# Optimization experiments

Hardware: AMD Instinct MI355X
Metric: run time of the kernel (lower is better)

## Reference

```python
import jax, jax.numpy as jnp
import numpy as np

B, T, H, NH = 4, 1024, 1024, 16
HS = H // NH
FF = 4 * H
EPS = 1e-5


def setup_inputs() -> dict:
    key = jax.random.key(0)
    ks = jax.random.split(key, 12)
    s = 0.02
    inp = {
        "x": jax.random.normal(ks[0], (B, T, H), jnp.float32),
        # attention projections, stored as [in, out] so y = x @ W + b
        "Wq": jax.random.normal(ks[1], (H, H), jnp.float32) * s,
        "bq": jnp.zeros((H,), jnp.float32),
        "Wk": jax.random.normal(ks[2], (H, H), jnp.float32) * s,
        "bk": jnp.zeros((H,), jnp.float32),
        "Wv": jax.random.normal(ks[3], (H, H), jnp.float32) * s,
        "bv": jnp.zeros((H,), jnp.float32),
        "Wo": jax.random.normal(ks[4], (H, H), jnp.float32) * s,
        "bo": jnp.zeros((H,), jnp.float32),
        # layernorms
        "ln1_w": jnp.ones((H,), jnp.float32),
        "ln1_b": jnp.zeros((H,), jnp.float32),
        "ln2_w": jnp.ones((H,), jnp.float32),
        "ln2_b": jnp.zeros((H,), jnp.float32),
        # MLP
        "Wfc": jax.random.normal(ks[5], (H, FF), jnp.float32) * s,
        "bfc": jnp.zeros((FF,), jnp.float32),
        "Wpr": jax.random.normal(ks[6], (FF, H), jnp.float32) * s,
        "bpr": jnp.zeros((H,), jnp.float32),
    }
    return inp


def _layernorm(x, w, b):
    mu = jnp.mean(x, axis=-1, keepdims=True)
    var = jnp.mean(jnp.square(x - mu), axis=-1, keepdims=True)
    return (x - mu) * jax.lax.rsqrt(var + EPS) * w + b


def _rope(x):
    # x: [B, nh, T, hs]; interleaved-pair RoPE, base 10000
    half = HS // 2
    inv_freq = 1.0 / (10000.0 ** (jnp.arange(half, dtype=jnp.float32) / half))
    ang = jnp.arange(T, dtype=jnp.float32)[:, None] * inv_freq[None, :]  # [T, half]
    cos, sin = jnp.cos(ang), jnp.sin(ang)
    xr = x.reshape(*x.shape[:-1], half, 2)
    x0, x1 = xr[..., 0], xr[..., 1]
    r0 = x0 * cos - x1 * sin
    r1 = x0 * sin + x1 * cos
    return jnp.stack([r0, r1], axis=-1).reshape(x.shape)


def _block(x, Wq, bq, Wk, bk, Wv, bv, Wo, bo, ln1_w, ln1_b, ln2_w, ln2_b, Wfc, bfc, Wpr, bpr):
    # --- attention sub-block ---
    h1 = _layernorm(x, ln1_w, ln1_b)
    q = (h1 @ Wq + bq).reshape(B, T, NH, HS).transpose(0, 2, 1, 3)  # [B,nh,T,hs]
    k = (h1 @ Wk + bk).reshape(B, T, NH, HS).transpose(0, 2, 1, 3)
    v = (h1 @ Wv + bv).reshape(B, T, NH, HS).transpose(0, 2, 1, 3)
    q, k = _rope(q), _rope(k)
    scores = jnp.einsum('bhqd,bhkd->bhqk', q, k) / jnp.sqrt(jnp.float32(HS))
    attn = jax.nn.softmax(scores, axis=-1)
    # NOTE: original applies the causal mask AFTER softmax (multiplicative, no renorm)
    causal = jnp.tril(jnp.ones((T, T), jnp.float32))[None, None]
    attn = attn * causal
    out = jnp.einsum('bhqk,bhkd->bhqd', attn, v)
    out = out.transpose(0, 2, 1, 3).reshape(B, T, H)
    x = x + (out @ Wo + bo)
    # --- MLP sub-block ---
    h2 = _layernorm(x, ln2_w, ln2_b)
    m = jax.nn.gelu(h2 @ Wfc + bfc, approximate=False)
    x = x + (m @ Wpr + bpr)
    return x


def reference(x, Wq, bq, Wk, bk, Wv, bv, Wo, bo, ln1_w, ln1_b, ln2_w, ln2_b, Wfc, bfc, Wpr, bpr):
    return _block(x, Wq, bq, Wk, bk, Wv, bv, Wo, bo, ln1_w, ln1_b, ln2_w, ln2_b, Wfc, bfc, Wpr, bpr)
```

## Files before the change

### kernel.cpp

```cpp
#include <hip/hip_runtime.h>
#include <hip/hip_bf16.h>

typedef unsigned short u16;
typedef __attribute__((ext_vector_type(8))) short bf16x8;
typedef __attribute__((ext_vector_type(4))) float f32x4;
typedef __attribute__((ext_vector_type(4))) unsigned short u16x4;

#define B_  4
#define T_  1024
#define H_  1024
#define NH_ 16
#define HS_ 64
#define FF_ 4096
#define M_  (B_*T_)
#define QKV_S 3072

__device__ __forceinline__ u16 f2bf(float f){
  union { float f; unsigned u; } v; v.f = f;
  unsigned r = v.u + 0x7fffu + ((v.u >> 16) & 1u);
  return (u16)(r >> 16);
}
__device__ __forceinline__ float bf2f(u16 h){
  union { unsigned u; float f; } v; v.u = ((unsigned)h) << 16;
  return v.f;
}
__device__ __forceinline__ unsigned pack2bf(float a, float b){
  __hip_bfloat162 h = __float22bfloat162_rn(make_float2(a, b));
  union { __hip_bfloat162 h; unsigned u; } c; c.h = h;
  return c.u;
}

__device__ __forceinline__ void gload_lds16(const void* g, void* l){
  __builtin_amdgcn_global_load_lds(
      (const __attribute__((address_space(1))) unsigned int*)g,
      (__attribute__((address_space(3))) unsigned int*)l,
      16, 0, 0);
}

__device__ __forceinline__ void trans_tile(const float* __restrict__ W,
                                           u16* __restrict__ Wt, int K, int N,
                                           int k0, int n0, int tid)
{
  __shared__ u16 tile[64][68];
  #pragma unroll
  for (int it = 0; it < 4; ++it){
    int ci = tid + it * 256;
    int kr = ci >> 4, nc = ci & 15;
    float4 f = *(const float4*)(W + (size_t)(k0 + kr) * N + n0 + nc * 4);
    tile[kr][nc*4+0] = f2bf(f.x);
    tile[kr][nc*4+1] = f2bf(f.y);
    tile[kr][nc*4+2] = f2bf(f.z);
    tile[kr][nc*4+3] = f2bf(f.w);
  }
  __syncthreads();
  #pragma unroll
  for (int it = 0; it < 4; ++it){
    int co = tid + it * 256;
    int nr = co >> 4, kc = co & 15;
    u16x4 o;
    o[0] = tile[kc*4+0][nr];
    o[1] = tile[kc*4+1][nr];
    o[2] = tile[kc*4+2][nr];
    o[3] = tile[kc*4+3][nr];
    *(u16x4*)(Wt + (size_t)(n0 + nr) * K + k0 + kc * 4) = o;
  }
}

__global__ __launch_bounds__(256) void trans_qkvo_k(
    const float* __restrict__ Wq, const float* __restrict__ Wk,
    const float* __restrict__ Wv, const float* __restrict__ Wo,
    u16* __restrict__ WqkvT, u16* __restrict__ WoT)
{
  const int z = blockIdx.z;
  const float* src = (z == 0) ? Wq : (z == 1) ? Wk : (z == 2) ? Wv : Wo;
  u16* dst = (z == 3) ? WoT : (WqkvT + (size_t)z * 1024 * 1024);
  trans_tile(src, dst, H_, H_, blockIdx.y * 64, blockIdx.x * 64, threadIdx.x);
}

__global__ __launch_bounds__(256) void transpose_cvt(const float* __restrict__ W,
                                                     u16* __restrict__ Wt, int K, int N)
{
  trans_tile(W, Wt, K, N, blockIdx.y * 64, blockIdx.x * 64, threadIdx.x);
}

__global__ __launch_bounds__(256) void vtrans_k(const u16* __restrict__ qkv,
                                                u16* __restrict__ vtg)
{
  __shared__ u16 tile[64][72];
  const int bh = blockIdx.y, tt = blockIdx.x * 64;
  const int b = bh >> 4, h = bh & 15;
  const size_t src = (size_t)b * T_ * QKV_S + h * HS_ + 2048;
  const int tid = threadIdx.x;
  #pragma unroll
  for (int it = 0; it < 2; ++it){
    int ci = tid + it * 256;
    int r = ci >> 3, c = ci & 7;
    bf16x8 vvv = *(const bf16x8*)(qkv + src + (size_t)(tt + r) * QKV_S + c * 8);
    *(bf16x8*)&tile[r][c * 8] = vvv;
  }
  __syncthreads();
  #pragma unroll
  for (int it = 0; it < 2; ++it){
    int co = tid + it * 256;
    int d = co >> 3, c = co & 7;
    bf16x8 ov;
    #pragma unroll
    for (int j = 0; j < 8; ++j) ov[j] = (short)tile[c * 8 + j][d];
    *(bf16x8*)(vtg + (size_t)bh * HS_ * T_ + (size_t)d * T_ + tt + c * 8) = ov;
  }
}

__global__ void prep_small_k(const float* __restrict__ a, const float* __restrict__ b,
                             const float* __restrict__ c, float* __restrict__ o,
                             float* __restrict__ tab){
  int i = blockIdx.x * 256 + threadIdx.x;
  if (i < QKV_S){
    o[i] = (i < 1024) ? a[i] : (i < 2048) ? b[i - 1024] : c[i - 2048];
  } else {
    int j = i - QKV_S;
    if (j < T_ * 32){
      int t = j >> 5, f = j & 31;
      float inv = powf(10000.0f, -(float)f * (1.0f / 32.0f));
      float ang = (float)t * inv;
      tab[j*2+0] = cosf(ang);
      tab[j*2+1] = sinf(ang);
    }
  }
}

__global__ void rope_apply_k(u16* __restrict__ qkv, const float* __restrict__ tab){
  int i = blockIdx.x * blockDim.x + threadIdx.x;
  if (i >= B_*T_*NH_*32) return;
  int pr = i & 31;
  int nh = (i >> 5) & (NH_ - 1);
  int bt = i >> 9;
  int t  = bt & (T_ - 1);
  size_t idx = (size_t)bt * QKV_S + nh * HS_ + pr * 2;
  float c = tab[(t*32 + pr)*2], s = tab[(t*32 + pr)*2 + 1];
  const float qs = 0.125f * 1.44269504f;
  {
    float x0 = bf2f(qkv[idx]), x1 = bf2f(qkv[idx+1]);
    qkv[idx]   = f2bf((x0 * c - x1 * s) * qs);
    qkv[idx+1] = f2bf((x0 * s + x1 * c) * qs);
  }
  {
    float x0 = bf2f(qkv[idx+1024]), x1 = bf2f(qkv[idx+1025]);
    qkv[idx+1024] = f2bf(x0 * c - x1 * s);
    qkv[idx+1025] = f2bf(x0 * s + x1 * c);
  }
}

__global__ __launch_bounds__(256) void ln_kernel(const float* __restrict__ x,
    const float* __restrict__ w, const float* __restrict__ bgain,
    u16* __restrict__ out)
{
  const int row = blockIdx.x;
  const int t = threadIdx.x;
  float4 vv = ((const float4*)(x + (size_t)row * H_))[t];
  float s  = vv.x + vv.y + vv.z + vv.w;
  float s2 = vv.x*vv.x + vv.y*vv.y + vv.z*vv.z + vv.w*vv.w;
  #pragma unroll
  for (int mm = 1; mm < 64; mm <<= 1){ s += __shfl_xor(s, mm); s2 += __shfl_xor(s2, mm); }
  __shared__ float red[8];
  int wid = t >> 6;
  if ((t & 63) == 0){ red[wid] = s; red[4 + wid] = s2; }
  __syncthreads();
  s  = red[0] + red[1] + red[2] + red[3];
  s2 = red[4] + red[5] + red[6] + red[7];
  float mu  = s * (1.0f / H_);
  float var = s2 * (1.0f / H_) - mu * mu;
  float rin = rsqrtf(var + 1e-5f);
  float4 wv = ((const float4*)w)[t];
  float4 bv = ((const float4*)bgain)[t];
  u16x4 ov;
  ov[0] = f2bf((vv.x - mu) * rin * wv.x + bv.x);
  ov[1] = f2bf((vv.y - mu) * rin * wv.y + bv.y);
  ov[2] = f2bf((vv.z - mu) * rin * wv.z + bv.z);
  ov[3] = f2bf((vv.w - mu) * rin * wv.w + bv.w);
  ((u16x4*)(out + (size_t)row * H_))[t] = ov;
}

template<int EPI, int RING>
__global__ __launch_bounds__(512) void gemm_kernel(
    const u16* __restrict__ A, const u16* __restrict__ Bt,
    const float* __restrict__ bias, const float* __restrict__ res,
    void* __restrict__ Cout, int M, int N, int K)
{
  __shared__ __attribute__((aligned(16))) u16 As[RING][128 * 32];
  __shared__ __attribute__((aligned(16))) u16 Bs[RING][128 * 32];
  const int tid  = threadIdx.x;
  const int lane = tid & 63;
  const int wid  = tid >> 6;
  const int wm = wid >> 2, wn = wid & 3;
  const int lrow = lane & 15, lkg = lane >> 4;

  const int gx  = gridDim.x;
  const int nwg = gx * gridDim.y;
  const int wg  = blockIdx.y * gx + blockIdx.x;
  const int nx  = nwg >> 3;
  const int swz = (wg & 7) * nx + (wg >> 3);
  const int m0 = (swz / gx) * 128, n0 = (swz % gx) * 128;

  const int srow = tid >> 2;
  const int sdc  = tid & 3;
  const int scs  = sdc ^ ((srow >> 1) & 3);

  const u16* Arow = A  + (size_t)(m0 + srow) * K + scs * 8;
  const u16* Brow = Bt + (size_t)(n0 + srow) * K + scs * 8;
  const int dd = (srow * 4 + sdc) * 8;

  int aoff[4], boff[2];
  #pragma unroll
  for (int mi = 0; mi < 4; ++mi){
    int r = wm*64 + mi*16 + lrow;
    aoff[mi] = (r*4 + (lkg ^ ((r >> 1) & 3))) * 16;
  }
  #pragma unroll
  for (int ni = 0; ni < 2; ++ni){
    int r = wn*32 + ni*16 + lrow;
    boff[ni] = (r*4 + (lkg ^ ((r >> 1) & 3))) * 16;
  }

  f32x4 acc[4][2] = {};
  const int NT = K >> 5;
  constexpr int DIST = RING - 1;

  #pragma unroll
  for (int s = 0; s < DIST; ++s){
    gload_lds16(Arow + (s << 5), &As[s][dd]);
    gload_lds16(Brow + (s << 5), &Bs[s][dd]);
  }

  int rs = 0, wsl = DIST;
  for (int t = 0; t < NT; ++t){
    int cnt = NT - 1 - t; if (cnt > DIST - 1) cnt = DIST - 1;
    if (cnt >= 4)      asm volatile("s_waitcnt vmcnt(8)" ::: "memory");
    else if (cnt == 3) asm volatile("s_waitcnt vmcnt(6)" ::: "memory");
    else if (cnt == 2) asm volatile("s_waitcnt vmcnt(4)" ::: "memory");
    else if (cnt == 1) asm volatile("s_waitcnt vmcnt(2)" ::: "memory");
    else               asm volatile("s_waitcnt vmcnt(0)" ::: "memory");
    __builtin_amdgcn_s_barrier();

    const char* Ab = (const char*)&As[rs][0];
    const char* Bb = (const char*)&Bs[rs][0];
    rs = (rs + 1 == RING) ? 0 : rs + 1;

    bf16x8 af[4], bfr[2];
    #pragma unroll
    for (int mi = 0; mi < 4; ++mi)
      af[mi] = *(const bf16x8*)(Ab + aoff[mi]);
    #pragma unroll
    for (int ni = 0; ni < 2; ++ni)
      bfr[ni] = *(const bf16x8*)(Bb + boff[ni]);
    __builtin_amdgcn_sched_barrier(0);

    if (t + DIST < NT){
      int k0 = (t + DIST) << 5;
      gload_lds16(Arow + k0, &As[wsl][dd]);
      gload_lds16(Brow + k0, &Bs[wsl][dd]);
    }
    wsl = (wsl + 1 == RING) ? 0 : wsl + 1;

    #pragma unroll
    for (int mi = 0; mi < 4; ++mi)
      #pragma unroll
      for (int ni = 0; ni < 2; ++ni)
        acc[mi][ni] = __builtin_amdgcn_mfma_f32_16x16x32_bf16(af[mi], bfr[ni], acc[mi][ni], 0, 0, 0);
  }

  #pragma unroll
  for (int mi = 0; mi < 4; ++mi){
    #pragma unroll
    for (int ni = 0; ni < 2; ++ni){
      int col = n0 + wn*32 + ni*16 + lrow;
      float bv = bias[col];
      #pragma unroll
      for (int r = 0; r < 4; ++r){
        int row = m0 + wm*64 + mi*16 + lkg*4 + r;
        float v = acc[mi][ni][r] + bv;
        if (EPI == 1){
          float u = 0.7978845608f * v + 0.0356774081f * v * v * v;
          float e = exp2f(u * 2.8853900818f);
          v = v - v / (e + 1.0f);
        }
        if (EPI == 2){
          ((float*)Cout)[(size_t)row * N + col] = v + res[(size_t)row * N + col];
        } else {
          ((u16*)Cout)[(size_t)row * N + col] = f2bf(v);
        }
      }
    }
  }
}

__global__ __launch_bounds__(512, 4) void attn_kernel(
    const u16* __restrict__ qkv, const u16* __restrict__ vtg,
    u16* __restrict__ out)
{
  __shared__ u16 K_lds[3][64 * 64];
  __shared__ u16 VT_lds[3][64 * 64];
  __shared__ u16 P_lds[8][16 * 64];
  const int tid = threadIdx.x, lane = tid & 63, w = tid >> 6;
  const int lrow = lane & 15, lkg = lane >> 4;
  const int q0 = blockIdx.x * 128;
  const int bh = blockIdx.y, b = bh >> 4, h = bh & 15;
  const size_t baseq  = (size_t)b * T_ * QKV_S + h * HS_;
  const size_t basek  = baseq + 1024;
  const size_t basevt = (size_t)bh * HS_ * T_;
  const size_t baseo  = (size_t)b * T_ * H_ + h * HS_;
  const int qg = q0 + w * 16 + lrow;

  bf16x8 qa[2];
  {
    const u16* qp = qkv + baseq + (size_t)qg * QKV_S + lkg * 8;
    qa[0] = *(const bf16x8*)qp;
    qa[1] = *(const bf16x8*)(qp + 32);
  }

  const int r0 = tid >> 3, c0 = tid & 7, g0 = c0 ^ (r0 & 7);
  const u16* kap = qkv + basek + (size_t)r0 * QKV_S + g0 * 8;
  const u16* vap = vtg + basevt + (size_t)r0 * T_ + g0 * 8;
  const int kd = tid * 8;

  f32x4 o[4] = {};
  float mrun = -1e30f, lrun = 0.f;

  #pragma unroll
  for (int s = 0; s < 2; ++s){
    gload_lds16(kap + (size_t)s * 64 * QKV_S, &K_lds[s][kd]);
    gload_lds16(vap + s * 64,                 &VT_lds[s][kd]);
  }

  int rs = 0, wsl = 2;
  for (int t = 0; t < 16; ++t){
    const int kt = t << 6;
    if (t < 15) asm volatile("s_waitcnt vmcnt(2)" ::: "memory");
    else        asm volatile("s_waitcnt vmcnt(0)" ::: "memory");
    __builtin_amdgcn_s_barrier();
    __builtin_amdgcn_sched_barrier(0);

    if (t + 2 < 16){
      gload_lds16(kap + (size_t)(t + 2) * 64 * QKV_S, &K_lds[wsl][kd]);
      gload_lds16(vap + (t + 2) * 64,                 &VT_lds[wsl][kd]);
    }
    wsl = (wsl + 1 == 3) ? 0 : wsl + 1;

    const u16* Kc  = K_lds[rs];
    const u16* VTc = VT_lds[rs];
    rs = (rs + 1 == 3) ? 0 : rs + 1;

    f32x4 s[4];
    __builtin_amdgcn_s_setprio(1);
    #pragma unroll
    for (int mi = 0; mi < 4; ++mi){
      f32x4 c = {};
      #pragma unroll
      for (int ss = 0; ss < 2; ++ss){
        int r = mi * 16 + lrow;
        int off = r * 128 + (((ss * 4 + lkg) ^ (r & 7)) * 16);
        bf16x8 kb = *(const bf16x8*)((const char*)Kc + off);
        c = __builtin_amdgcn_mfma_f32_16x16x32_bf16(kb, qa[ss], c, 0, 0, 0);
      }
      s[mi] = c;
    }
    __builtin_amdgcn_s_setprio(0);

    float mt = fmaxf(fmaxf(fmaxf(s[0][0], s[0][1]), fmaxf(s[0][2], s[0][3])),
                     fmaxf(fmaxf(s[1][0], s[1][1]), fmaxf(s[1][2], s[1][3])));
    mt = fmaxf(mt, fmaxf(fmaxf(fmaxf(s[2][0], s[2][1]), fmaxf(s[2][2], s[2][3])),
                         fmaxf(fmaxf(s[3][0], s[3][1]), fmaxf(s[3][2], s[3][3]))));
    mt = fmaxf(mt, __shfl_xor(mt, 16));
    mt = fmaxf(mt, __shfl_xor(mt, 32));
    if (!__all(mt <= mrun + 8.f)){
      float mnew = fmaxf(mrun, mt);
      float fsc = exp2f(mrun - mnew);
      lrun *= fsc;
      #pragma unroll
      for (int nf = 0; nf < 4; ++nf){
        #pragma unroll
        for (int r = 0; r < 4; ++r) o[nf][r] *= fsc;
      }
      mrun = mnew;
    }

    float p[16];
    float ls = 0.f;
    #pragma unroll
    for (int mi = 0; mi < 4; ++mi){
      #pragma unroll
      for (int r = 0; r < 4; ++r){
        int key = kt + mi * 16 + lkg * 4 + r;
        float pv = exp2f(s[mi][r] - mrun);
        ls += pv;
        p[mi * 4 + r] = (key <= qg) ? pv : 0.f;
      }
    }
    ls += __shfl_xor(ls, 16);
    ls += __shfl_xor(ls, 32);
    lrun += ls;

    if (kt <= q0 + w * 16 + 15){
      char* pbase = (char*)&P_lds[w][0];
      const int rx = (lrow & 7) << 4;
      #pragma unroll
      for (int mi = 0; mi < 4; ++mi){
        uint2 pk;
        pk.x = pack2bf(p[mi*4+0], p[mi*4+1]);
        pk.y = pack2bf(p[mi*4+2], p[mi*4+3]);
        *(uint2*)(pbase + (lrow * 128 + ((mi * 32 + lkg * 8) ^ rx))) = pk;
      }
      __builtin_amdgcn_s_setprio(1);
      #pragma unroll
      for (int ss = 0; ss < 2; ++ss){
        bf16x8 pb = *(const bf16x8*)(pbase + (lrow * 128 + ((ss * 64 + lkg * 16) ^ rx)));
        #pragma unroll
        for (int nfd = 0; nfd < 4; ++nfd){
          int d = nfd * 16 + lrow;
          int off = d * 128 + (((ss * 4 + lkg) ^ (d & 7)) * 16);
          bf16x8 vb = *(const bf16x8*)((const char*)VTc + off);
          o[nfd] = __builtin_amdgcn_mfma_f32_16x16x32_bf16(vb, pb, o[nfd], 0, 0, 0);
        }
      }
      __builtin_amdgcn_s_setprio(0);
    }
  }

  float rl = 1.0f / lrun;
  #pragma unroll
  for (int nfd = 0; nfd < 4; ++nfd){
    uint2 ov;
    ov.x = pack2bf(o[nfd][0] * rl, o[nfd][1] * rl);
    ov.y = pack2bf(o[nfd][2] * rl, o[nfd][3] * rl);
    *(uint2*)(out + baseo + (size_t)qg * H_ + nfd * 16 + lkg * 4) = ov;
  }
}

extern "C" void kernel_launch(void* const* d_in, const int* in_sizes, int n_in,
                              void* d_out, int out_size, void* d_ws, size_t ws_size,
                              hipStream_t stream)
{
  (void)in_sizes; (void)n_in; (void)out_size; (void)ws_size;
  const float* x    = (const float*)d_in[0];
  const float* Wq   = (const float*)d_in[1];
  const float* bq   = (const float*)d_in[2];
  const float* Wk   = (const float*)d_in[3];
  const float* bk   = (const float*)d_in[4];
  const float* Wv   = (const float*)d_in[5];
  const float* bv   = (const float*)d_in[6];
  const float* Wo   = (const float*)d_in[7];
  const float* bo   = (const float*)d_in[8];
  const float* ln1w = (const float*)d_in[9];
  const float* ln1b = (const float*)d_in[10];
  const float* ln2w = (const float*)d_in[11];
  const float* ln2b = (const float*)d_in[12];
  const float* Wfc  = (const float*)d_in[13];
  const float* bfc  = (const float*)d_in[14];
  const float* Wpr  = (const float*)d_in[15];
  const float* bpr  = (const float*)d_in[16];

  char* ws = (char*)d_ws;
  u16*  WqkvT = (u16*)(ws + ((size_t) 0 << 20));
  u16*  WoT   = (u16*)(ws + ((size_t) 6 << 20));
  u16*  WfcT  = (u16*)(ws + ((size_t) 8 << 20));
  u16*  WprT  = (u16*)(ws + ((size_t)16 << 20));
  u16*  h1    = (u16*)(ws + ((size_t)24 << 20));
  u16*  qkvb  = (u16*)(ws + ((size_t)32 << 20));
  float* x1   = (float*)(ws + ((size_t)32 << 20));
  u16*  h2    = (u16*)(ws + ((size_t)48 << 20));
  float* bqkv = (float*)(ws + ((size_t)56 << 20));
  float* rtab = (float*)(ws + ((size_t)56 << 20) + (64 << 10));
  u16*  vtg   = (u16*)(ws + ((size_t)57 << 20));
  u16*  mb    = (u16*)(ws + ((size_t)56 << 20));
  u16*  attnout = h1;

  dim3 blk(256);
  dim3 gblk(512);

  trans_qkvo_k<<<dim3(H_/64, H_/64, 4), blk, 0, stream>>>(Wq, Wk, Wv, Wo, WqkvT, WoT);
  transpose_cvt<<<dim3(FF_/64, H_/64),  blk, 0, stream>>>(Wfc, WfcT, H_,  FF_);
  transpose_cvt<<<dim3(H_/64,  FF_/64), blk, 0, stream>>>(Wpr, WprT, FF_, H_);
  prep_small_k<<<dim3((QKV_S + T_*32 + 255)/256), blk, 0, stream>>>(bq, bk, bv, bqkv, rtab);

  ln_kernel<<<dim3(M_), blk, 0, stream>>>(x, ln1w, ln1b, h1);
  gemm_kernel<0,3><<<dim3(QKV_S/128, M_/128), gblk, 0, stream>>>(h1, WqkvT, bqkv, nullptr, qkvb, M_, QKV_S, H_);
  rope_apply_k<<<dim3((B_*T_*NH_*32)/256), blk, 0, stream>>>(qkvb, rtab);
  vtrans_k<<<dim3(T_/64, B_*NH_), blk, 0, stream>>>(qkvb, vtg);
  attn_kernel<<<dim3(T_/128, B_*NH_), dim3(512), 0, stream>>>(qkvb, vtg, attnout);
  gemm_kernel<2,6><<<dim3(H_/128, M_/128), gblk, 0, stream>>>(attnout, WoT, bo, x, x1, M_, H_, H_);
  ln_kernel<<<dim3(M_), blk, 0, stream>>>(x1, ln2w, ln2b, h2);
  gemm_kernel<1,3><<<dim3(FF_/128, M_/128), gblk, 0, stream>>>(h2, WfcT, bfc, nullptr, mb, M_, FF_, H_);
  gemm_kernel<2,6><<<dim3(H_/128, M_/128), gblk, 0, stream>>>(mb, WprT, bpr, x1, (float*)d_out, M_, H_, FF_);
}
```

Measured before the change: 254.0 us.

## Add 128x256-tile GEMM with vectorized bf16 epilogue for QKV and FC layers

Adds a new GEMM kernel whose workgroup tile is 128x256 instead of 128x128. Each of its 8 waves computes a 64x64 sub-tile and the kernel uses a 3-stage LDS ring with K-step 32. It also adds a workgroup-index swizzle and an epilogue that adds bias as float4 and writes packed bf16x4 stores. The QKV and FC GEMMs now use it, which is meant to raise arithmetic intensity per byte loaded and cut global-load traffic for the wider-N matrices. The cost is more LDS and registers per workgroup and fewer workgroups in the grid, which may hurt occupancy or wave balance.

```diff
diff --git a/kernel.cpp b/kernel.cpp
--- a/kernel.cpp
+++ b/kernel.cpp
@@ -293,6 +293,125 @@
   }
 }
 
+template<int EPI>
+__global__ __launch_bounds__(512, 4) void gemm256_kernel(
+    const u16* __restrict__ A, const u16* __restrict__ Bt,
+    const float* __restrict__ bias,
+    void* __restrict__ Cout, int M, int N, int K)
+{
+  __shared__ __attribute__((aligned(16))) u16 As[3][128 * 32];
+  __shared__ __attribute__((aligned(16))) u16 Bs[3][256 * 32];
+  const int tid  = threadIdx.x;
+  const int lane = tid & 63;
+  const int wid  = tid >> 6;
+  const int wm = wid >> 2, wn = wid & 3;
+  const int lrow = lane & 15, lkg = lane >> 4;
+
+  const int gx  = gridDim.x;
+  const int nwg = gx * gridDim.y;
+  const int wg  = blockIdx.y * gx + blockIdx.x;
+  const int nx  = nwg >> 3;
+  const int swz = (wg & 7) * nx + (wg >> 3);
+  const int m0 = (swz / gx) * 128, n0 = (swz % gx) * 256;
+
+  const int srow = tid >> 2;
+  const int sdc  = tid & 3;
+  const int scs  = sdc ^ ((srow >> 1) & 3);
+  const u16* Asrc  = A  + (size_t)(m0 + srow) * K + scs * 8;
+  const u16* Bsrc0 = Bt + (size_t)(n0 + srow) * K + scs * 8;
+  const u16* Bsrc1 = Bsrc0 + (size_t)128 * K;
+  const int dA  = (srow * 4 + sdc) * 8;
+  const int dB1 = dA + 128 * 32;
+
+  int aoff[4], boff[4];
+  #pragma unroll
+  for (int mi = 0; mi < 4; ++mi){
+    int r = wm*64 + mi*16 + lrow;
+    aoff[mi] = (r*4 + (lkg ^ ((r >> 1) & 3))) * 16;
+  }
+  #pragma unroll
+  for (int ni = 0; ni < 4; ++ni){
+    int r = wn*64 + ni*16 + lrow;
+    boff[ni] = (r*4 + (lkg ^ ((r >> 1) & 3))) * 16;
+  }
+
+  f32x4 acc[4][4] = {};
+  const int NT = K >> 5;
+
+  #pragma unroll
+  for (int s = 0; s < 2; ++s){
+    gload_lds16(Asrc  + (s << 5), &As[s][dA]);
+    gload_lds16(Bsrc0 + (s << 5), &Bs[s][dA]);
+    gload_lds16(Bsrc1 + (s << 5), &Bs[s][dB1]);
+  }
+
+  int rs = 0, wsl = 2;
+  for (int t = 0; t < NT; ++t){
+    if (t < NT - 1) asm volatile("s_waitcnt vmcnt(3)" ::: "memory");
+    else            asm volatile("s_waitcnt vmcnt(0)" ::: "memory");
+    __builtin_amdgcn_s_barrier();
+
+    const char* Ab = (const char*)&As[rs][0];
+    const char* Bb = (const char*)&Bs[rs][0];
+    rs = (rs + 1 == 3) ? 0 : rs + 1;
+
+    bf16x8 af[4], bfr[4];
+    #pragma unroll
+    for (int mi = 0; mi < 4; ++mi)
+      af[mi] = *(const bf16x8*)(Ab + aoff[mi]);
+    #pragma unroll
+    for (int ni = 0; ni < 4; ++ni)
+      bfr[ni] = *(const bf16x8*)(Bb + boff[ni]);
+    __builtin_amdgcn_sched_barrier(0);
+
+    if (t + 2 < NT){
+      int k0 = (t + 2) << 5;
+      gload_lds16(Asrc  + k0, &As[wsl][dA]);
+      gload_lds16(Bsrc0 + k0, &Bs[wsl][dA]);
+      gload_lds16(Bsrc1 + k0, &Bs[wsl][dB1]);
+    }
+    wsl = (wsl + 1 == 3) ? 0 : wsl + 1;
+
+    #pragma unroll
+    for (int mi = 0; mi < 4; ++mi)
+      #pragma unroll
+      for (int ni = 0; ni < 4; ++ni)
+        acc[mi][ni] = __builtin_amdgcn_mfma_f32_16x16x32_bf16(bfr[ni], af[mi], acc[mi][ni], 0, 0, 0);
+  }
+
+  #pragma unroll
+  for (int mi = 0; mi < 4; ++mi){
+    int row = m0 + wm*64 + mi*16 + lrow;
+    #pragma unroll
+    for (int ni = 0; ni < 4; ++ni){
+      int col0 = n0 + wn*64 + ni*16 + lkg*4;
+      float4 bv = *(const float4*)(bias + col0);
+      float v0 = acc[mi][ni][0] + bv.x;
+      float v1 = acc[mi][ni][1] + bv.y;
+      float v2 = acc[mi][ni][2] + bv.z;
+      float v3 = acc[mi][ni][3] + bv.w;
+      if (EPI == 1){
+        float u0 = 0.7978845608f * v0 + 0.0356774081f * v0 * v0 * v0;
+        float u1 = 0.7978845608f * v1 + 0.0356774081f * v1 * v1 * v1;
+        float u2 = 0.7978845608f * v2 + 0.0356774081f * v2 * v2 * v2;
+        float u3 = 0.7978845608f * v3 + 0.0356774081f * v3 * v3 * v3;
+        float e0 = exp2f(u0 * 2.8853900818f);
+        float e1 = exp2f(u1 * 2.8853900818f);
+        float e2 = exp2f(u2 * 2.8853900818f);
+        float e3 = exp2f(u3 * 2.8853900818f);
+        v0 = v0 - v0 / (e0 + 1.0f);
+        v1 = v1 - v1 / (e1 + 1.0f);
+        v2 = v2 - v2 / (e2 + 1.0f);
+        v3 = v3 - v3 / (e3 + 1.0f);
+      }
+      uint2 ov;
+      ov.x = pack2bf(v0, v1);
+      ov.y = pack2bf(v2, v3);
+      *(uint2*)((u16*)Cout + (size_t)row * N + col0) = ov;
+    }
+  }
+}
+
 __global__ __launch_bounds__(512, 4) void attn_kernel(
     const u16* __restrict__ qkv, const u16* __restrict__ vtg,
     u16* __restrict__ out)
@@ -482,12 +601,12 @@
   prep_small_k<<<dim3((QKV_S + T_*32 + 255)/256), blk, 0, stream>>>(bq, bk, bv, bqkv, rtab);
 
   ln_kernel<<<dim3(M_), blk, 0, stream>>>(x, ln1w, ln1b, h1);
-  gemm_kernel<0,3><<<dim3(QKV_S/128, M_/128), gblk, 0, stream>>>(h1, WqkvT, bqkv, nullptr, qkvb, M_, QKV_S, H_);
+  gemm256_kernel<0><<<dim3(QKV_S/256, M_/128), gblk, 0, stream>>>(h1, WqkvT, bqkv, qkvb, M_, QKV_S, H_);
   rope_apply_k<<<dim3((B_*T_*NH_*32)/256), blk, 0, stream>>>(qkvb, rtab);
   vtrans_k<<<dim3(T_/64, B_*NH_), blk, 0, stream>>>(qkvb, vtg);
   attn_kernel<<<dim3(T_/128, B_*NH_), dim3(512), 0, stream>>>(qkvb, vtg, attnout);
   gemm_kernel<2,6><<<dim3(H_/128, M_/128), gblk, 0, stream>>>(attnout, WoT, bo, x, x1, M_, H_, H_);
   ln_kernel<<<dim3(M_), blk, 0, stream>>>(x1, ln2w, ln2b, h2);
-  gemm_kernel<1,3><<<dim3(FF_/128, M_/128), gblk, 0, stream>>>(h2, WfcT, bfc, nullptr, mb, M_, FF_, H_);
+  gemm256_kernel<1><<<dim3(FF_/256, M_/128), gblk, 0, stream>>>(h2, WfcT, bfc, mb, M_, FF_, H_);
   gemm_kernel<2,6><<<dim3(H_/128, M_/128), gblk, 0, stream>>>(mb, WprT, bpr, x1, (float*)d_out, M_, H_, FF_);
 }
```

Measured after the change: 256.5 us. Within noise of the previous version (+1.0%).
